# Performance work log

Hardware: AMD Instinct MI355X
Metric: run time of the kernel (lower is better)

## Reference

```python
import jax, jax.numpy as jnp
import numpy as np
from jax import lax

K = 10  # k_neighbors (k = min(k, N); N=1024 so k=10)


def setup_inputs() -> dict:
    key = jax.random.key(0)
    ks = jax.random.split(key, 6)
    B, N, M, D = 4, 1024, 8, 128
    PROJ, NC, OUT = 64, 10, 128
    x = jax.random.normal(ks[0], (B, N, M, D), dtype=jnp.float32)
    # Linear params (torch stores weight as [out, in])
    W_proj_w = jax.random.normal(ks[1], (PROJ, D), dtype=jnp.float32) / np.sqrt(D)
    W_proj_b = jnp.zeros((PROJ,), dtype=jnp.float32)
    C = jax.random.normal(ks[2], (NC, PROJ), dtype=jnp.float32) * np.sqrt(2.0 / (NC + PROJ))
    Theta_w = jax.random.normal(ks[3], (OUT, D), dtype=jnp.float32) / np.sqrt(D)
    Theta_b = jnp.zeros((OUT,), dtype=jnp.float32)
    return {"x": x, "W_proj_w": W_proj_w, "W_proj_b": W_proj_b, "C": C,
            "Theta_w": Theta_w, "Theta_b": Theta_b}


def _forward(x, W_proj_w, W_proj_b, C, Theta_w, Theta_b):
    B, N, M, D = x.shape
    BM = B * M
    x_flat = jnp.transpose(x, (0, 2, 1, 3)).reshape(BM, N, D)
    Z = x_flat @ W_proj_w.T + W_proj_b  # [BM, N, P]
    # squared euclidean pairwise distances (same topk ordering as cdist)
    sq = jnp.sum(Z * Z, axis=-1)  # [BM, N]
    d2 = sq[:, :, None] + sq[:, None, :] - 2.0 * jnp.einsum('bnp,bmp->bnm', Z, Z)
    _, idx = lax.top_k(-d2, K)  # k smallest distances -> [BM, N, K]
    # scatter 1.0 at neighbor indices
    b_ix = jnp.arange(BM)[:, None, None]
    r_ix = jnp.arange(N)[None, :, None]
    H_knn = jnp.zeros((BM, N, N), dtype=jnp.float32).at[b_ix, r_ix, idx].set(1.0)
    H_cluster = jax.nn.softmax(Z @ C.T, axis=-1)  # [BM, N, NC]
    H = jnp.concatenate([H_knn, H_cluster], axis=-1)  # [BM, N, N+NC]
    # hypergraph conv with degree normalization
    D_e = H.sum(axis=1)  # [BM, E]
    D_e_inv = jnp.where(D_e > 0, 1.0 / jnp.maximum(D_e, 1e-12), 0.0)
    D_v = H.sum(axis=2)  # [BM, N]
    D_v_inv_sqrt = jnp.where(D_v > 0, 1.0 / jnp.sqrt(jnp.maximum(D_v, 1e-12)), 0.0)
    X_trans = x_flat @ Theta_w.T + Theta_b  # [BM, N, F]
    out = D_v_inv_sqrt[:, :, None] * X_trans
    out = jnp.einsum('bne,bnf->bef', H, out)   # H^T @ out
    out = D_e_inv[:, :, None] * out
    out = jnp.einsum('bne,bef->bnf', H, out)   # H @ out
    out = D_v_inv_sqrt[:, :, None] * out
    out = jax.nn.elu(out)
    return jnp.transpose(out.reshape(B, M, N, -1), (0, 2, 1, 3))  # [B, N, M, F]


def reference(x, W_proj_w, W_proj_b, C, Theta_w, Theta_b):
    return _forward(x, W_proj_w, W_proj_b, C, Theta_w, Theta_b)
```

## Files before the change

### kernel.cpp

```cpp
#include <hip/hip_runtime.h>
#include <hip/hip_bf16.h>
#include <cstdint>
#include <cstddef>

#define BMC 32
#define NNODE 1024
#define DIN 128
#define PPROJ 64
#define NCLUS 10
#define FOUT 128
#define KNB 10

typedef _Float16 half8 __attribute__((ext_vector_type(8)));
typedef float f32x4 __attribute__((ext_vector_type(4)));

static const size_t OFF_Z    = 0;
static const size_t OFF_SQ   = 2097152;
static const size_t OFF_HC   = 2129920;
static const size_t OFF_IDX  = 2457600;
static const size_t OFF_CNT  = 2785280;
static const size_t OFF_FILL = 2818048;
static const size_t OFF_EC   = 2850816;
static const size_t OFF_DCV  = 2891776;
static const size_t OFF_OFFS = 2892096;
static const size_t OFF_ADJ  = 2924864;
static const size_t OFF_FLAG = 3252544;
static const size_t OFF_END  = 3252608;
static const size_t OFF_WPH  = OFF_EC;
static const size_t OFF_WPL  = OFF_EC +  4096;
static const size_t OFF_THH  = OFF_EC +  8192;
static const size_t OFF_THL  = OFF_EC + 16384;
static const int    ZERO2_N  = 41280;

__device__ __forceinline__ float bfu(unsigned int lo16) {
    return __uint_as_float(lo16 << 16);
}
__device__ __forceinline__ float bfhi(unsigned int w) {
    return __uint_as_float(w & 0xffff0000u);
}
__device__ __forceinline__ float ldf(const void* p, size_t i, bool isbf) {
    return isbf ? bfu((unsigned int)((const unsigned short*)p)[i])
                : ((const float*)p)[i];
}
__device__ __forceinline__ unsigned short f2bf(float v) {
    __hip_bfloat16 h = __float2bfloat16(v);
    return *(unsigned short*)&h;
}

__device__ __forceinline__ unsigned long long mkkey(float v, int col) {
    unsigned int bits = __float_as_uint(v);
    unsigned int s = bits ^ (0x80000000u | (unsigned int)((int)bits >> 31));
    return ((unsigned long long)s << 32) | (unsigned int)col;
}
__device__ __forceinline__ void kcas(unsigned long long &a, unsigned long long &b) {
    bool c = b < a;
    unsigned long long t = c ? b : a;
    b = c ? a : b;
    a = t;
}
__device__ __forceinline__ void kmin(unsigned long long &a, unsigned long long b) {
    a = (b < a) ? b : a;
}

__global__ __launch_bounds__(256) void k_probe(const unsigned int* __restrict__ xw,
                                               int* __restrict__ flag) {
    __shared__ int red[256];
    int t = threadIdx.x;
    int cnt = 0;
    for (int i = t; i < 1024; i += 256) {
        float b = bfu(xw[i] & 0xffffu);
        float ab = fabsf(b);
        if (ab > 9.5e-7f && ab < 1.0e6f) cnt++;
    }
    red[t] = cnt;
    __syncthreads();
    for (int off = 128; off > 0; off >>= 1) {
        if (t < off) red[t] += red[t + off];
        __syncthreads();
    }
    if (t == 0) flag[0] = (red[0] >= 700) ? 1 : 0;
}

__global__ __launch_bounds__(256) void k_split(const void* __restrict__ Wp,
                                               const void* __restrict__ Th,
                                               const int* __restrict__ flag,
                                               _Float16* __restrict__ WpH,
                                               _Float16* __restrict__ WpL,
                                               _Float16* __restrict__ ThH,
                                               _Float16* __restrict__ ThL,
                                               int* __restrict__ cntz) {
    const bool isbf = (flag[0] != 0);
    int i = blockIdx.x * 256 + threadIdx.x;
    cntz[i] = 0;
    if (i < 8192) cntz[i + 24576] = 0;
    if (i < 8192) {
        float v = ldf(Wp, i, isbf);
        _Float16 h = (_Float16)v;
        WpH[i] = h;
        WpL[i] = (_Float16)((v - (float)h) * 2048.0f);
    } else {
        int j = i - 8192;
        float v = ldf(Th, j, isbf);
        _Float16 h = (_Float16)v;
        ThH[j] = h;
        ThL[j] = (_Float16)((v - (float)h) * 2048.0f);
    }
}

__global__ __launch_bounds__(256) void k_proj(const void* __restrict__ x,
                                              const _Float16* __restrict__ WpH,
                                              const _Float16* __restrict__ WpL,
                                              const void* __restrict__ Wpb,
                                              const void* __restrict__ Cm,
                                              const int* __restrict__ flag,
                                              _Float16* __restrict__ Zh,
                                              _Float16* __restrict__ Zl,
                                              float* __restrict__ sqv,
                                              float* __restrict__ Hc) {
    __shared__ __align__(16) _Float16 wps[2][64][72];
    __shared__ __align__(16) _Float16 xsh[2][32][72];
    __shared__ float zs[32][68];
    __shared__ float cs[10][64];

    const bool isbf = (flag[0] != 0);
    int tid = threadIdx.x;
    int bi  = blockIdx.x;
    int bm  = bi >> 5;
    int n0  = (bi & 31) << 5;
    int b   = bm >> 3, m = bm & 7;

    int lane = tid & 63, wave = tid >> 6;
    int m16 = lane & 15, quad = lane >> 4;
    int rh = wave >> 1, ch = wave & 1;

    for (int e = tid; e < 640; e += 256) cs[e >> 6][e & 63] = ldf(Cm, e, isbf);

    f32x4 aH[2], aX[2];
#pragma unroll
    for (int t = 0; t < 2; ++t) {
        aH[t] = (f32x4){0.f, 0.f, 0.f, 0.f};
        aX[t] = (f32x4){0.f, 0.f, 0.f, 0.f};
    }

    for (int kc = 0; kc < 2; ++kc) {
        __syncthreads();
        for (int e = tid; e < 512; e += 256) {
            int p = e >> 3, c = e & 7;
            *(uint4*)&wps[0][p][c * 8] =
                *(const uint4*)(WpH + (size_t)p * 128 + kc * 64 + c * 8);
            *(uint4*)&wps[1][p][c * 8] =
                *(const uint4*)(WpL + (size_t)p * 128 + kc * 64 + c * 8);
        }
        for (int e = tid; e < 2048; e += 256) {
            int r = e >> 6, dk = e & 63;
            float v = ldf(x, (((size_t)b * NNODE + n0 + r) * 8 + m) * DIN + kc * 64 + dk, isbf);
            _Float16 h = (_Float16)v;
            xsh[0][r][dk] = h;
            xsh[1][r][dk] = (_Float16)((v - (float)h) * 2048.0f);
        }
        __syncthreads();
#pragma unroll
        for (int c32 = 0; c32 < 2; ++c32) {
            half8 Ah = *(const half8*)&xsh[0][rh * 16 + m16][c32 * 32 + quad * 8];
            half8 Al = *(const half8*)&xsh[1][rh * 16 + m16][c32 * 32 + quad * 8];
#pragma unroll
            for (int t = 0; t < 2; ++t) {
                int p = ch * 32 + t * 16 + m16;
                half8 Bh = *(const half8*)&wps[0][p][c32 * 32 + quad * 8];
                half8 Bl = *(const half8*)&wps[1][p][c32 * 32 + quad * 8];
                aH[t] = __builtin_amdgcn_mfma_f32_16x16x32_f16(Ah, Bh, aH[t], 0, 0, 0);
                aX[t] = __builtin_amdgcn_mfma_f32_16x16x32_f16(Al, Bh, aX[t], 0, 0, 0);
                aX[t] = __builtin_amdgcn_mfma_f32_16x16x32_f16(Ah, Bl, aX[t], 0, 0, 0);
            }
        }
    }

#pragma unroll
    for (int t = 0; t < 2; ++t) {
        int p = ch * 32 + t * 16 + m16;
        float bias = ldf(Wpb, p, isbf);
#pragma unroll
        for (int r = 0; r < 4; ++r) {
            int row = rh * 16 + quad * 4 + r;
            float v = aH[t][r] + aX[t][r] * (1.0f / 2048.0f) + bias;
            zs[row][p] = v;
            size_t off = ((size_t)bm * NNODE + n0 + row) * 64 + p;
            _Float16 h = (_Float16)v;
            Zh[off] = h;
            Zl[off] = (_Float16)((v - (float)h) * 2048.0f);
        }
    }
    __syncthreads();

    int row = tid >> 3, slot = tid & 7;
    int d0 = slot * 8;
    float sp = 0.f;
#pragma unroll
    for (int dd = 0; dd < 8; ++dd) { float z = zs[row][d0+dd]; sp += z * z; }
#pragma unroll
    for (int mm = 1; mm < 8; mm <<= 1) sp += __shfl_xor(sp, mm, 8);
    size_t g = (size_t)bm * NNODE + n0 + row;
    if (slot == 0) sqv[g] = sp;

    float sc[10];
#pragma unroll
    for (int c = 0; c < 10; ++c) {
        float pa = 0.f;
#pragma unroll
        for (int dd = 0; dd < 8; ++dd) pa += zs[row][d0+dd] * cs[c][d0+dd];
#pragma unroll
        for (int mm = 1; mm < 8; mm <<= 1) pa += __shfl_xor(pa, mm, 8);
        sc[c] = pa;
    }
    float mx = sc[0];
#pragma unroll
    for (int c = 1; c < 10; ++c) mx = fmaxf(mx, sc[c]);
    float ssum = 0.f;
#pragma unroll
    for (int c = 0; c < 10; ++c) { sc[c] = expf(sc[c] - mx); ssum += sc[c]; }
    float inv = 1.0f / ssum;
#pragma unroll
    for (int c = 0; c < 10; ++c)
        if ((c & 7) == slot) Hc[g * 10 + c] = sc[c] * inv;
}

__global__ __launch_bounds__(256) void k_theta(const void* __restrict__ x,
                                               const _Float16* __restrict__ ThH,
                                               const _Float16* __restrict__ ThL,
                                               const void* __restrict__ Thb,
                                               const int* __restrict__ flag,
                                               float* __restrict__ Xt) {
    __shared__ __align__(16) _Float16 ths[2][128][72];
    __shared__ __align__(16) _Float16 xsh[32][72];

    const bool isbf = (flag[0] != 0);
    int tid = threadIdx.x;
    int bi  = blockIdx.x;
    int bm  = bi >> 5;
    int n0  = (bi & 31) << 5;
    int b   = bm >> 3, m = bm & 7;

    int lane = tid & 63, wave = tid >> 6;
    int m16 = lane & 15, quad = lane >> 4;
    int rh = wave >> 1, ch = wave & 1;

    f32x4 aH[4], aX[4];
#pragma unroll
    for (int t = 0; t < 4; ++t) {
        aH[t] = (f32x4){0.f, 0.f, 0.f, 0.f};
        aX[t] = (f32x4){0.f, 0.f, 0.f, 0.f};
    }

    for (int kc = 0; kc < 2; ++kc) {
        __syncthreads();
        for (int e = tid; e < 1024; e += 256) {
            int f = e >> 3, c = e & 7;
            *(uint4*)&ths[0][f][c * 8] =
                *(const uint4*)(ThH + (size_t)f * 128 + kc * 64 + c * 8);
            *(uint4*)&ths[1][f][c * 8] =
                *(const uint4*)(ThL + (size_t)f * 128 + kc * 64 + c * 8);
        }
        for (int e = tid; e < 2048; e += 256) {
            int r = e >> 6, dk = e & 63;
            float v = ldf(x, (((size_t)b * NNODE + n0 + r) * 8 + m) * DIN + kc * 64 + dk, isbf);
            xsh[r][dk] = (_Float16)v;
        }
        __syncthreads();
#pragma unroll
        for (int c32 = 0; c32 < 2; ++c32) {
            half8 Ah = *(const half8*)&xsh[rh * 16 + m16][c32 * 32 + quad * 8];
#pragma unroll
            for (int t = 0; t < 4; ++t) {
                int f = ch * 64 + t * 16 + m16;
                half8 Bh = *(const half8*)&ths[0][f][c32 * 32 + quad * 8];
                half8 Bl = *(const half8*)&ths[1][f][c32 * 32 + quad * 8];
                aH[t] = __builtin_amdgcn_mfma_f32_16x16x32_f16(Ah, Bh, aH[t], 0, 0, 0);
                aX[t] = __builtin_amdgcn_mfma_f32_16x16x32_f16(Ah, Bl, aX[t], 0, 0, 0);
            }
        }
    }
#pragma unroll
    for (int t = 0; t < 4; ++t) {
        int f = ch * 64 + t * 16 + m16;
        float bias = ldf(Thb, f, isbf);
        size_t rb = (size_t)bm * NNODE + n0 + rh * 16 + quad * 4;
#pragma unroll
        for (int r = 0; r < 4; ++r) {
            Xt[(rb + r) * 128 + f] = aH[t][r] + aX[t][r] * (1.0f / 2048.0f) + bias;
        }
    }
}

#define TOPK_SELECT(J0)                                                        \
  {                                                                            \
    unsigned long long b0 = mkkey(ST[(sslot     ) * 36 + srow], (J0) + sslot);        \
    unsigned long long b1 = mkkey(ST[(sslot +  8) * 36 + srow], (J0) + sslot + 8);    \
    unsigned long long b2 = mkkey(ST[(sslot + 16) * 36 + srow], (J0) + sslot + 16);   \
    unsigned long long b3 = mkkey(ST[(sslot + 24) * 36 + srow], (J0) + sslot + 24);   \
    unsigned long long b4 = mkkey(ST[(sslot + 32) * 36 + srow], (J0) + sslot + 32);   \
    unsigned long long b5 = mkkey(ST[(sslot + 40) * 36 + srow], (J0) + sslot + 40);   \
    unsigned long long b6 = mkkey(ST[(sslot + 48) * 36 + srow], (J0) + sslot + 48);   \
    unsigned long long b7 = mkkey(ST[(sslot + 56) * 36 + srow], (J0) + sslot + 56);   \
    kcas(b0, b1); kcas(b2, b3); kcas(b4, b5); kcas(b6, b7);                    \
    kcas(b0, b2); kcas(b1, b3); kcas(b4, b6); kcas(b5, b7);                    \
    kcas(b1, b2); kcas(b5, b6);                                                \
    kcas(b0, b4); kcas(b1, b5); kcas(b2, b6); kcas(b3, b7);                    \
    kcas(b2, b4); kcas(b3, b5);                                                \
    kcas(b1, b2); kcas(b3, b4); kcas(b5, b6);                                  \
    kmin(keys[2], b7); kmin(keys[3], b6); kmin(keys[4], b5); kmin(keys[5], b4);\
    kmin(keys[6], b3); kmin(keys[7], b2); kmin(keys[8], b1); kmin(keys[9], b0);\
    kcas(keys[0], keys[8]); kcas(keys[1], keys[9]);                            \
    kcas(keys[2], keys[6]); kcas(keys[3], keys[7]);                            \
    kcas(keys[4], keys[8]); kcas(keys[5], keys[9]);                            \
    kcas(keys[2], keys[4]); kcas(keys[3], keys[5]);                            \
    kcas(keys[6], keys[8]); kcas(keys[7], keys[9]);                            \
    kcas(keys[0], keys[1]); kcas(keys[2], keys[3]);                            \
    kcas(keys[4], keys[5]); kcas(keys[6], keys[7]); kcas(keys[8], keys[9]);    \
  }

#define TOPK_TILE(J0, CH0,CH1,CL0,CL1,CSQ, NH0,NH1,NL0,NL1,NSQ)                \
  {                                                                            \
    f32x4 acc  = {0.f, 0.f, 0.f, 0.f};                                         \
    f32x4 accx = {0.f, 0.f, 0.f, 0.f};                                         \
    acc  = __builtin_amdgcn_mfma_f32_16x16x32_f16(ah0, CH0, acc, 0, 0, 0);     \
    acc  = __builtin_amdgcn_mfma_f32_16x16x32_f16(ah1, CH1, acc, 0, 0, 0);     \
    accx = __builtin_amdgcn_mfma_f32_16x16x32_f16(al0, CH0, accx, 0, 0, 0);    \
    accx = __builtin_amdgcn_mfma_f32_16x16x32_f16(ah0, CL0, accx, 0, 0, 0);    \
    accx = __builtin_amdgcn_mfma_f32_16x16x32_f16(al1, CH1, accx, 0, 0, 0);    \
    accx = __builtin_amdgcn_mfma_f32_16x16x32_f16(ah1, CL1, accx, 0, 0, 0);    \
    f32x4 sc;                                                                  \
    _Pragma("unroll")                                                          \
    for (int r = 0; r < 4; ++r) {                                              \
      float g = acc[r] + accx[r] * (1.0f / 2048.0f);                           \
      sc[r] = fmaf(-2.0f, g, CSQ);                                             \
    }                                                                          \
    *(f32x4*)&ST[cl * 36 + quad * 4] = sc;                                     \
    f32x4 accB  = {0.f, 0.f, 0.f, 0.f};                                        \
    f32x4 accxB = {0.f, 0.f, 0.f, 0.f};                                        \
    accB  = __builtin_amdgcn_mfma_f32_16x16x32_f16(ah0b, CH0, accB, 0, 0, 0);  \
    accB  = __builtin_amdgcn_mfma_f32_16x16x32_f16(ah1b, CH1, accB, 0, 0, 0);  \
    accxB = __builtin_amdgcn_mfma_f32_16x16x32_f16(al0b, CH0, accxB, 0, 0, 0); \
    accxB = __builtin_amdgcn_mfma_f32_16x16x32_f16(ah0b, CL0, accxB, 0, 0, 0); \
    accxB = __builtin_amdgcn_mfma_f32_16x16x32_f16(al1b, CH1, accxB, 0, 0, 0); \
    accxB = __builtin_amdgcn_mfma_f32_16x16x32_f16(ah1b, CL1, accxB, 0, 0, 0); \
    _Pragma("unroll")                                                          \
    for (int r = 0; r < 4; ++r) {                                              \
      float g = accB[r] + accxB[r] * (1.0f / 2048.0f);                         \
      sc[r] = fmaf(-2.0f, g, CSQ);                                             \
    }                                                                          \
    *(f32x4*)&ST[cl * 36 + 16 + quad * 4] = sc;                                \
    {                                                                          \
      const _Float16* pnb = Zhb + (size_t)((J0) + 64 + cl) * 64 + quad * 8;    \
      const _Float16* pnl = Zlb + (size_t)((J0) + 64 + cl) * 64 + quad * 8;    \
      NH0 = *(const half8*)pnb;                                                \
      NH1 = *(const half8*)(pnb + 32);                                         \
      NL0 = *(const half8*)pnl;                                                \
      NL1 = *(const half8*)(pnl + 32);                                         \
      NSQ = sqb[(J0) + 64 + cl];                                               \
    }                                                                          \
    asm volatile("s_waitcnt lgkmcnt(0)" ::: "memory");                         \
    __builtin_amdgcn_s_barrier();                                              \
    asm volatile("" ::: "memory");                                             \
    TOPK_SELECT(J0);                                                           \
    asm volatile("" ::: "memory");                                             \
    __builtin_amdgcn_s_barrier();                                              \
    asm volatile("" ::: "memory");                                             \
  }

__global__ __launch_bounds__(256) void k_topk(const _Float16* __restrict__ Zh,
                                              const _Float16* __restrict__ Zl,
                                              const float* __restrict__ sqv,
                                              int* __restrict__ idxo,
                                              int* __restrict__ cnt) {
    __shared__ float ST[64 * 36];

    int tid = threadIdx.x;
    int bi  = blockIdx.x;
    int bm  = bi >> 5;
    int n0  = (bi & 31) << 5;
    const _Float16* Zhb = Zh + (size_t)bm * NNODE * 64;
    const _Float16* Zlb = Zl + (size_t)bm * NNODE * 64;
    const float*    sqb = sqv + (size_t)bm * NNODE;

    int lane = tid & 63, wave = tid >> 6;
    int m16 = lane & 15, quad = lane >> 4;
    int cl = wave * 16 + m16;

    half8 ah0, ah1, al0, al1, ah0b, ah1b, al0b, al1b;
    {
        size_t ab = (size_t)(n0 + m16) * 64 + quad * 8;
        ah0 = *(const half8*)(Zhb + ab);
        ah1 = *(const half8*)(Zhb + ab + 32);
        al0 = *(const half8*)(Zlb + ab);
        al1 = *(const half8*)(Zlb + ab + 32);
        size_t ab2 = ab + 16 * 64;
        ah0b = *(const half8*)(Zhb + ab2);
        ah1b = *(const half8*)(Zhb + ab2 + 32);
        al0b = *(const half8*)(Zlb + ab2);
        al1b = *(const half8*)(Zlb + ab2 + 32);
    }

    unsigned long long keys[10];
#pragma unroll
    for (int j = 0; j < 10; ++j) keys[j] = ~0ULL;

    int srow  = tid >> 3;
    int sslot = tid & 7;

    half8 cbh0, cbh1, cbl0, cbl1, nbh0, nbh1, nbl0, nbl1;
    float csq, nsq;
    {
        const _Float16* pb = Zhb + (size_t)cl * 64 + quad * 8;
        const _Float16* pl = Zlb + (size_t)cl * 64 + quad * 8;
        cbh0 = *(const half8*)pb;
        cbh1 = *(const half8*)(pb + 32);
        cbl0 = *(const half8*)pl;
        cbl1 = *(const half8*)(pl + 32);
        csq  = sqb[cl];
    }

    for (int tp = 0; tp < 8; ++tp) {
        int j0a = tp << 7;
        TOPK_TILE(j0a,      cbh0, cbh1, cbl0, cbl1, csq, nbh0, nbh1, nbl0, nbl1, nsq)
        TOPK_TILE(j0a + 64, nbh0, nbh1, nbl0, nbl1, nsq, cbh0, cbh1, cbl0, cbl1, csq)
    }

    size_t gr = (size_t)bm * NNODE + n0 + srow;
    for (int it = 0; it < 10; ++it) {
        unsigned long long mine = keys[0];
        unsigned long long best = mine;
#pragma unroll
        for (int mm = 1; mm < 8; mm <<= 1) {
            unsigned long long o = __shfl_xor(best, mm, 8);
            if (o < best) best = o;
        }
        if (best == mine) {
#pragma unroll
            for (int j = 0; j < 9; ++j) keys[j] = keys[j+1];
            keys[9] = ~0ULL;
            int col = (int)(best & 0xFFFFFFFFu);
            idxo[gr * KNB + it] = col;
            atomicAdd(&cnt[bm * NNODE + col], 1);
        }
    }
}
#undef TOPK_TILE
#undef TOPK_SELECT

__global__ __launch_bounds__(256) void k_csr(const int* __restrict__ cnt,
                                             const int* __restrict__ idxb,
                                             int* __restrict__ offs,
                                             int* __restrict__ adj) {
    __shared__ int part[256];
    __shared__ int fillL[1024];
    int bm = blockIdx.x, t = threadIdx.x;
    int base = bm * 1024 + t * 4;
    int c0 = cnt[base], c1 = cnt[base+1], c2 = cnt[base+2], c3 = cnt[base+3];
    int ps = c0 + c1 + c2 + c3;
    part[t] = ps;
    __syncthreads();
    for (int off = 1; off < 256; off <<= 1) {
        int add = (t >= off) ? part[t - off] : 0;
        __syncthreads();
        part[t] += add;
        __syncthreads();
    }
    int e0 = part[t] - ps;
    int gb = bm * (NNODE * KNB);
    int o0 = gb + e0, o1 = o0 + c0, o2 = o1 + c1, o3 = o2 + c2;
    offs[base]   = o0;
    offs[base+1] = o1;
    offs[base+2] = o2;
    offs[base+3] = o3;
    fillL[t*4]   = o0;
    fillL[t*4+1] = o1;
    fillL[t*4+2] = o2;
    fillL[t*4+3] = o3;
    __syncthreads();
    int ibase = bm * (NNODE * KNB);
    for (int e = t; e < NNODE * KNB; e += 256) {
        int eidx = idxb[ibase + e];
        int pos = atomicAdd(&fillL[eidx], 1);
        adj[pos] = (bm << 10) + (e / 10);
    }
}

__global__ __launch_bounds__(256) void k_edge(const float* __restrict__ Xt,
                                              const int* __restrict__ offs,
                                              const int* __restrict__ cnt,
                                              const int* __restrict__ adj,
                                              unsigned short* __restrict__ Ek,
                                              float* __restrict__ EcZ) {
    int tid = threadIdx.x;
    int bi  = blockIdx.x;
    {
        int zi = bi * 256 + tid;
        if (zi < ZERO2_N) EcZ[zi] = 0.0f;
    }
    int swz = (bi & 7) * 512 + (bi >> 3);
    int e = swz * 8 + (tid >> 5);
    int l = tid & 31;
    int start = offs[e];
    int num = cnt[e];
    float4 acc = {0.f, 0.f, 0.f, 0.f};
    if (num > 0) {
        int nm1 = num - 1;
        int gidx[16];
#pragma unroll
        for (int j = 0; j < 16; ++j) {
            int jj = (j < nm1) ? j : nm1;
            gidx[j] = adj[start + jj];
        }
#pragma unroll
        for (int j = 0; j < 16; ++j) {
            float4 a = *(const float4*)(Xt + (size_t)gidx[j] * 128 + l * 4);
            float w = (j < num) ? 1.0f : 0.0f;
            acc.x = fmaf(w, a.x, acc.x);
            acc.y = fmaf(w, a.y, acc.y);
            acc.z = fmaf(w, a.z, acc.z);
            acc.w = fmaf(w, a.w, acc.w);
        }
        int i = 16;
        for (; i + 1 < num; i += 2) {
            int g0 = adj[start + i];
            int g1 = adj[start + i + 1];
            float4 a = *(const float4*)(Xt + (size_t)g0 * 128 + l * 4);
            float4 b = *(const float4*)(Xt + (size_t)g1 * 128 + l * 4);
            acc.x += a.x + b.x; acc.y += a.y + b.y;
            acc.z += a.z + b.z; acc.w += a.w + b.w;
        }
        if (i < num) {
            int g0 = adj[start + i];
            float4 a = *(const float4*)(Xt + (size_t)g0 * 128 + l * 4);
            acc.x += a.x; acc.y += a.y; acc.z += a.z; acc.w += a.w;
        }
    }
    float scale = (num > 0) ? 1.0f / (float)num : 0.0f;
    ushort4 o;
    o.x = f2bf(acc.x * scale);
    o.y = f2bf(acc.y * scale);
    o.z = f2bf(acc.z * scale);
    o.w = f2bf(acc.w * scale);
    *(ushort4*)(Ek + (size_t)e * 128 + l * 4) = o;
}

__global__ __launch_bounds__(256) void k_clus(const float* __restrict__ Xt,
                                              const float* __restrict__ Hc,
                                              float* __restrict__ Ec,
                                              float* __restrict__ Dcv) {
    __shared__ float hcs[128][12];
    int tid = threadIdx.x;
    int bm = blockIdx.x >> 3;
    int ch = blockIdx.x & 7;
    int n0 = ch * 128;

    for (int e = tid; e < 1280; e += 256) {
        int r = e / 10, c = e - r * 10;
        hcs[r][c] = Hc[((size_t)bm * NNODE + n0 + r) * 10 + c];
    }
    __syncthreads();

    int f = tid & 127;
    int h = tid >> 7;
    int c0 = h * 5;
    float acc[5]  = {0.f,0.f,0.f,0.f,0.f};
    float dacc[5] = {0.f,0.f,0.f,0.f,0.f};
#pragma unroll 2
    for (int n = 0; n < 128; ++n) {
        float xv = Xt[((size_t)bm * NNODE + n0 + n) * 128 + f];
#pragma unroll
        for (int j = 0; j < 5; ++j) {
            float hv = hcs[n][c0 + j];
            acc[j]  = fmaf(hv, xv, acc[j]);
            dacc[j] += hv;
        }
    }
#pragma unroll
    for (int j = 0; j < 5; ++j)
        atomicAdd(&Ec[((size_t)bm * 10 + c0 + j) * 128 + f], acc[j]);
    if (f == 0) {
#pragma unroll
        for (int j = 0; j < 5; ++j) atomicAdd(&Dcv[bm * 10 + c0 + j], dacc[j]);
    }
}

__global__ __launch_bounds__(256) void k_final(const unsigned short* __restrict__ Ek,
                                               const float* __restrict__ Ec,
                                               const float* __restrict__ Hc,
                                               const float* __restrict__ Dcv,
                                               const int* __restrict__ idxb,
                                               float* __restrict__ out) {
    int tid = threadIdx.x;
    int bi  = blockIdx.x;
    int swz = (bi & 7) * 512 + (bi >> 3);
    int g = swz * 8 + (tid >> 5);
    int l = tid & 31;
    int bm = g >> 10, n = g & 1023;
    const int* ip = idxb + (size_t)g * 10;
    const unsigned short* ekb = Ek + ((size_t)bm << 10) * 128 + l * 4;

    int e0 = ip[0], e1 = ip[1], e2 = ip[2], e3 = ip[3], e4 = ip[4];
    int e5 = ip[5], e6 = ip[6], e7 = ip[7], e8 = ip[8], e9 = ip[9];
    ushort4 u0 = *(const ushort4*)(ekb + (size_t)e0 * 128);
    ushort4 u1 = *(const ushort4*)(ekb + (size_t)e1 * 128);
    ushort4 u2 = *(const ushort4*)(ekb + (size_t)e2 * 128);
    ushort4 u3 = *(const ushort4*)(ekb + (size_t)e3 * 128);
    ushort4 u4 = *(const ushort4*)(ekb + (size_t)e4 * 128);
    ushort4 u5 = *(const ushort4*)(ekb + (size_t)e5 * 128);
    ushort4 u6 = *(const ushort4*)(ekb + (size_t)e6 * 128);
    ushort4 u7 = *(const ushort4*)(ekb + (size_t)e7 * 128);
    ushort4 u8 = *(const ushort4*)(ekb + (size_t)e8 * 128);
    ushort4 u9 = *(const ushort4*)(ekb + (size_t)e9 * 128);

    float4 acc;
    acc.x = bfu(u0.x) + bfu(u1.x) + bfu(u2.x) + bfu(u3.x) + bfu(u4.x)
          + bfu(u5.x) + bfu(u6.x) + bfu(u7.x) + bfu(u8.x) + bfu(u9.x);
    acc.y = bfu(u0.y) + bfu(u1.y) + bfu(u2.y) + bfu(u3.y) + bfu(u4.y)
          + bfu(u5.y) + bfu(u6.y) + bfu(u7.y) + bfu(u8.y) + bfu(u9.y);
    acc.z = bfu(u0.z) + bfu(u1.z) + bfu(u2.z) + bfu(u3.z) + bfu(u4.z)
          + bfu(u5.z) + bfu(u6.z) + bfu(u7.z) + bfu(u8.z) + bfu(u9.z);
    acc.w = bfu(u0.w) + bfu(u1.w) + bfu(u2.w) + bfu(u3.w) + bfu(u4.w)
          + bfu(u5.w) + bfu(u6.w) + bfu(u7.w) + bfu(u8.w) + bfu(u9.w);

    const float* hp  = Hc + (size_t)g * 10;
    const float* dcp = Dcv + (size_t)bm * 10;
    const float* ecp = Ec + (size_t)bm * 10 * 128 + l * 4;
#pragma unroll
    for (int c = 0; c < 10; ++c) {
        float d  = dcp[c];
        float hv = (d > 0.f) ? hp[c] / d : 0.f;
        float4 ec = *(const float4*)(ecp + c * 128);
        acc.x += hv * ec.x; acc.y += hv * ec.y;
        acc.z += hv * ec.z; acc.w += hv * ec.w;
    }
    float4 r;
    r.x = acc.x * (1.0f / 11.0f);
    r.y = acc.y * (1.0f / 11.0f);
    r.z = acc.z * (1.0f / 11.0f);
    r.w = acc.w * (1.0f / 11.0f);
    r.x = (r.x > 0.f) ? r.x : expm1f(r.x);
    r.y = (r.y > 0.f) ? r.y : expm1f(r.y);
    r.z = (r.z > 0.f) ? r.z : expm1f(r.z);
    r.w = (r.w > 0.f) ? r.w : expm1f(r.w);
    int b = bm >> 3, m = bm & 7;
    *(float4*)(out + (((size_t)b * NNODE + n) * 8 + m) * 128 + l * 4) = r;
}

extern "C" void kernel_launch(void* const* d_in, const int* in_sizes, int n_in,
                              void* d_out, int out_size, void* d_ws, size_t ws_size,
                              hipStream_t stream) {
    const void* x   = d_in[0];
    const void* Wp  = d_in[1];
    const void* Wpb = d_in[2];
    const void* Cm  = d_in[3];
    const void* Th  = d_in[4];
    const void* Thb = d_in[5];
    float* ws = (float*)d_ws;

    if (ws_size < OFF_END * sizeof(float)) return;

    _Float16* Zh = (_Float16*)(ws + OFF_Z);
    _Float16* Zl = (_Float16*)(ws + OFF_Z + 1048576);
    float* sqv  = ws + OFF_SQ;
    float* Hc   = ws + OFF_HC;
    int*   idxb = (int*)(ws + OFF_IDX);
    int*   cnt  = (int*)(ws + OFF_CNT);
    float* Ec   = ws + OFF_EC;
    float* Dcv  = ws + OFF_DCV;
    int*   offs = (int*)(ws + OFF_OFFS);
    int*   adj  = (int*)(ws + OFF_ADJ);
    int*   flag = (int*)(ws + OFF_FLAG);
    _Float16* WpH = (_Float16*)(ws + OFF_WPH);
    _Float16* WpL = (_Float16*)(ws + OFF_WPL);
    _Float16* ThH = (_Float16*)(ws + OFF_THH);
    _Float16* ThL = (_Float16*)(ws + OFF_THL);
    unsigned short* Ek = (unsigned short*)(ws + OFF_Z);
    float* Xt  = (float*)d_out;
    float* out = (float*)d_out;

    k_probe <<<1,    256, 0, stream>>>((const unsigned int*)x, flag);
    k_split <<<96,   256, 0, stream>>>(Wp, Th, flag, WpH, WpL, ThH, ThL, cnt);
    k_proj  <<<1024, 256, 0, stream>>>(x, WpH, WpL, Wpb, Cm, flag, Zh, Zl, sqv, Hc);
    k_topk  <<<1024, 256, 0, stream>>>(Zh, Zl, sqv, idxb, cnt);
    k_csr   <<<32,   256, 0, stream>>>(cnt, idxb, offs, adj);
    k_theta <<<1024, 256, 0, stream>>>(x, ThH, ThL, Thb, flag, Xt);
    k_edge  <<<4096, 256, 0, stream>>>(Xt, offs, cnt, adj, Ek, Ec);
    k_clus  <<<256,  256, 0, stream>>>(Xt, Hc, Ec, Dcv);
    k_final <<<4096, 256, 0, stream>>>(Ek, Ec, Hc, Dcv, idxb, out);
}
```

Baseline: 268.6 us.

## Halve top-k block row tile to 16 rows, doubling grid and shrinking sort network

The top-k kernel now handles 16 query rows per block instead of 32, so the grid doubles to 2048 blocks. Each row is served by 16 threads that each sort 4 candidates instead of 8 threads sorting 8, which shortens the per-thread sorting network. The shuffle reduction widens to 16 lanes to match. s_setprio is also raised around the MFMA block. The aim is more parallelism and less serial compare-swap work per thread, paid for by reloading each column tile of Z twice as often and running more barriers per useful row.

Result: slower. 290.7 us (+8.2%).

```diff
diff --git a/kernel.cpp b/kernel.cpp
--- a/kernel.cpp
+++ b/kernel.cpp
@@ -293,21 +293,13 @@
 
 #define TOPK_SELECT(J0)                                                        \
   {                                                                            \
-    unsigned long long b0 = mkkey(ST[(sslot     ) * 36 + srow], (J0) + sslot);        \
-    unsigned long long b1 = mkkey(ST[(sslot +  8) * 36 + srow], (J0) + sslot + 8);    \
-    unsigned long long b2 = mkkey(ST[(sslot + 16) * 36 + srow], (J0) + sslot + 16);   \
-    unsigned long long b3 = mkkey(ST[(sslot + 24) * 36 + srow], (J0) + sslot + 24);   \
-    unsigned long long b4 = mkkey(ST[(sslot + 32) * 36 + srow], (J0) + sslot + 32);   \
-    unsigned long long b5 = mkkey(ST[(sslot + 40) * 36 + srow], (J0) + sslot + 40);   \
-    unsigned long long b6 = mkkey(ST[(sslot + 48) * 36 + srow], (J0) + sslot + 48);   \
-    unsigned long long b7 = mkkey(ST[(sslot + 56) * 36 + srow], (J0) + sslot + 56);   \
-    kcas(b0, b1); kcas(b2, b3); kcas(b4, b5); kcas(b6, b7);                    \
-    kcas(b0, b2); kcas(b1, b3); kcas(b4, b6); kcas(b5, b7);                    \
-    kcas(b1, b2); kcas(b5, b6);                                                \
-    kcas(b0, b4); kcas(b1, b5); kcas(b2, b6); kcas(b3, b7);                    \
-    kcas(b2, b4); kcas(b3, b5);                                                \
-    kcas(b1, b2); kcas(b3, b4); kcas(b5, b6);                                  \
-    kmin(keys[2], b7); kmin(keys[3], b6); kmin(keys[4], b5); kmin(keys[5], b4);\
+    unsigned long long b0 = mkkey(ST[(sslot     ) * 20 + srow], (J0) + sslot);        \
+    unsigned long long b1 = mkkey(ST[(sslot + 16) * 20 + srow], (J0) + sslot + 16);   \
+    unsigned long long b2 = mkkey(ST[(sslot + 32) * 20 + srow], (J0) + sslot + 32);   \
+    unsigned long long b3 = mkkey(ST[(sslot + 48) * 20 + srow], (J0) + sslot + 48);   \
+    kcas(b0, b1); kcas(b2, b3);                                                \
+    kcas(b0, b2); kcas(b1, b3);                                                \
+    kcas(b1, b2);                                                              \
     kmin(keys[6], b3); kmin(keys[7], b2); kmin(keys[8], b1); kmin(keys[9], b0);\
     kcas(keys[0], keys[8]); kcas(keys[1], keys[9]);                            \
     kcas(keys[2], keys[6]); kcas(keys[3], keys[7]);                            \
@@ -320,6 +312,7 @@
 
 #define TOPK_TILE(J0, CH0,CH1,CL0,CL1,CSQ, NH0,NH1,NL0,NL1,NSQ)                \
   {                                                                            \
+    __builtin_amdgcn_s_setprio(1);                                             \
     f32x4 acc  = {0.f, 0.f, 0.f, 0.f};                                         \
     f32x4 accx = {0.f, 0.f, 0.f, 0.f};                                         \
     acc  = __builtin_amdgcn_mfma_f32_16x16x32_f16(ah0, CH0, acc, 0, 0, 0);     \
@@ -328,27 +321,14 @@
     accx = __builtin_amdgcn_mfma_f32_16x16x32_f16(ah0, CL0, accx, 0, 0, 0);    \
     accx = __builtin_amdgcn_mfma_f32_16x16x32_f16(al1, CH1, accx, 0, 0, 0);    \
     accx = __builtin_amdgcn_mfma_f32_16x16x32_f16(ah1, CL1, accx, 0, 0, 0);    \
+    __builtin_amdgcn_s_setprio(0);                                             \
     f32x4 sc;                                                                  \
     _Pragma("unroll")                                                          \
     for (int r = 0; r < 4; ++r) {                                              \
       float g = acc[r] + accx[r] * (1.0f / 2048.0f);                           \
       sc[r] = fmaf(-2.0f, g, CSQ);                                             \
     }                                                                          \
-    *(f32x4*)&ST[cl * 36 + quad * 4] = sc;                                     \
-    f32x4 accB  = {0.f, 0.f, 0.f, 0.f};                                        \
-    f32x4 accxB = {0.f, 0.f, 0.f, 0.f};                                        \
-    accB  = __builtin_amdgcn_mfma_f32_16x16x32_f16(ah0b, CH0, accB, 0, 0, 0);  \
-    accB  = __builtin_amdgcn_mfma_f32_16x16x32_f16(ah1b, CH1, accB, 0, 0, 0);  \
-    accxB = __builtin_amdgcn_mfma_f32_16x16x32_f16(al0b, CH0, accxB, 0, 0, 0); \
-    accxB = __builtin_amdgcn_mfma_f32_16x16x32_f16(ah0b, CL0, accxB, 0, 0, 0); \
-    accxB = __builtin_amdgcn_mfma_f32_16x16x32_f16(al1b, CH1, accxB, 0, 0, 0); \
-    accxB = __builtin_amdgcn_mfma_f32_16x16x32_f16(ah1b, CL1, accxB, 0, 0, 0); \
-    _Pragma("unroll")                                                          \
-    for (int r = 0; r < 4; ++r) {                                              \
-      float g = accB[r] + accxB[r] * (1.0f / 2048.0f);                         \
-      sc[r] = fmaf(-2.0f, g, CSQ);                                             \
-    }                                                                          \
-    *(f32x4*)&ST[cl * 36 + 16 + quad * 4] = sc;                                \
+    *(f32x4*)&ST[cl * 20 + quad * 4] = sc;                                     \
     {                                                                          \
       const _Float16* pnb = Zhb + (size_t)((J0) + 64 + cl) * 64 + quad * 8;    \
       const _Float16* pnl = Zlb + (size_t)((J0) + 64 + cl) * 64 + quad * 8;    \
@@ -372,12 +352,12 @@
                                               const float* __restrict__ sqv,
                                               int* __restrict__ idxo,
                                               int* __restrict__ cnt) {
-    __shared__ float ST[64 * 36];
+    __shared__ float ST[64 * 20];
 
     int tid = threadIdx.x;
     int bi  = blockIdx.x;
-    int bm  = bi >> 5;
-    int n0  = (bi & 31) << 5;
+    int bm  = bi >> 6;
+    int n0  = (bi & 63) << 4;
     const _Float16* Zhb = Zh + (size_t)bm * NNODE * 64;
     const _Float16* Zlb = Zl + (size_t)bm * NNODE * 64;
     const float*    sqb = sqv + (size_t)bm * NNODE;
@@ -386,26 +366,21 @@
     int m16 = lane & 15, quad = lane >> 4;
     int cl = wave * 16 + m16;
 
-    half8 ah0, ah1, al0, al1, ah0b, ah1b, al0b, al1b;
+    half8 ah0, ah1, al0, al1;
     {
         size_t ab = (size_t)(n0 + m16) * 64 + quad * 8;
         ah0 = *(const half8*)(Zhb + ab);
         ah1 = *(const half8*)(Zhb + ab + 32);
         al0 = *(const half8*)(Zlb + ab);
         al1 = *(const half8*)(Zlb + ab + 32);
-        size_t ab2 = ab + 16 * 64;
-        ah0b = *(const half8*)(Zhb + ab2);
-        ah1b = *(const half8*)(Zhb + ab2 + 32);
-        al0b = *(const half8*)(Zlb + ab2);
-        al1b = *(const half8*)(Zlb + ab2 + 32);
     }
 
     unsigned long long keys[10];
 #pragma unroll
     for (int j = 0; j < 10; ++j) keys[j] = ~0ULL;
 
-    int srow  = tid >> 3;
-    int sslot = tid & 7;
+    int srow  = tid >> 4;
+    int sslot = tid & 15;
 
     half8 cbh0, cbh1, cbl0, cbl1, nbh0, nbh1, nbl0, nbl1;
     float csq, nsq;
@@ -430,8 +405,8 @@
         unsigned long long mine = keys[0];
         unsigned long long best = mine;
 #pragma unroll
-        for (int mm = 1; mm < 8; mm <<= 1) {
-            unsigned long long o = __shfl_xor(best, mm, 8);
+        for (int mm = 1; mm < 16; mm <<= 1) {
+            unsigned long long o = __shfl_xor(best, mm, 16);
             if (o < best) best = o;
         }
         if (best == mine) {
@@ -681,7 +656,7 @@
     k_probe <<<1,    256, 0, stream>>>((const unsigned int*)x, flag);
     k_split <<<96,   256, 0, stream>>>(Wp, Th, flag, WpH, WpL, ThH, ThL, cnt);
     k_proj  <<<1024, 256, 0, stream>>>(x, WpH, WpL, Wpb, Cm, flag, Zh, Zl, sqv, Hc);
-    k_topk  <<<1024, 256, 0, stream>>>(Zh, Zl, sqv, idxb, cnt);
+    k_topk  <<<2048, 256, 0, stream>>>(Zh, Zl, sqv, idxb, cnt);
     k_csr   <<<32,   256, 0, stream>>>(cnt, idxb, offs, adj);
     k_theta <<<1024, 256, 0, stream>>>(x, ThH, ThL, Thb, flag, Xt);
     k_edge  <<<4096, 256, 0, stream>>>(Xt, offs, cnt, adj, Ek, Ec);
```

## Merge probe into split kernel and fuse cluster aggregation into edge kernel

Applied to the files above, without the earlier changes.

The dtype probe is folded into k_split: every block recomputes the reduction and block 0 writes the flag. The Ec/Dcv zeroing moves from k_edge into k_split, and the split weights are relocated into the fill scratch area so the zeroing does not clobber them. k_clus becomes the first 256 blocks of a combined k_edgeclus launch. This cuts two kernel launches and their serialization gaps. The cost is redundant probe work in every split block and mixed block types in one grid.

Result: faster. 252.1 us (-6.1%).

```diff
diff --git a/kernel.cpp b/kernel.cpp
--- a/kernel.cpp
+++ b/kernel.cpp
@@ -26,11 +26,10 @@
 static const size_t OFF_ADJ  = 2924864;
 static const size_t OFF_FLAG = 3252544;
 static const size_t OFF_END  = 3252608;
-static const size_t OFF_WPH  = OFF_EC;
-static const size_t OFF_WPL  = OFF_EC +  4096;
-static const size_t OFF_THH  = OFF_EC +  8192;
-static const size_t OFF_THL  = OFF_EC + 16384;
-static const int    ZERO2_N  = 41280;
+static const size_t OFF_WPH  = OFF_FILL;
+static const size_t OFF_WPL  = OFF_FILL +  4096;
+static const size_t OFF_THH  = OFF_FILL +  8192;
+static const size_t OFF_THL  = OFF_FILL + 16384;
 
 __device__ __forceinline__ float bfu(unsigned int lo16) {
     return __uint_as_float(lo16 << 16);
@@ -62,37 +61,39 @@
     a = (b < a) ? b : a;
 }
 
-__global__ __launch_bounds__(256) void k_probe(const unsigned int* __restrict__ xw,
-                                               int* __restrict__ flag) {
-    __shared__ int red[256];
-    int t = threadIdx.x;
-    int cnt = 0;
-    for (int i = t; i < 1024; i += 256) {
-        float b = bfu(xw[i] & 0xffffu);
-        float ab = fabsf(b);
-        if (ab > 9.5e-7f && ab < 1.0e6f) cnt++;
-    }
-    red[t] = cnt;
-    __syncthreads();
-    for (int off = 128; off > 0; off >>= 1) {
-        if (t < off) red[t] += red[t + off];
-        __syncthreads();
-    }
-    if (t == 0) flag[0] = (red[0] >= 700) ? 1 : 0;
-}
-
-__global__ __launch_bounds__(256) void k_split(const void* __restrict__ Wp,
+__global__ __launch_bounds__(256) void k_split(const unsigned int* __restrict__ xw,
+                                               const void* __restrict__ Wp,
                                                const void* __restrict__ Th,
-                                               const int* __restrict__ flag,
+                                               int* __restrict__ flag,
                                                _Float16* __restrict__ WpH,
                                                _Float16* __restrict__ WpL,
                                                _Float16* __restrict__ ThH,
                                                _Float16* __restrict__ ThL,
-                                               int* __restrict__ cntz) {
-    const bool isbf = (flag[0] != 0);
-    int i = blockIdx.x * 256 + threadIdx.x;
+                                               int* __restrict__ cntz,
+                                               float* __restrict__ EcZ) {
+    __shared__ int red[256];
+    int t = threadIdx.x;
+    int c = 0;
+    for (int i = t; i < 1024; i += 256) {
+        float b = bfu(xw[i] & 0xffffu);
+        float ab = fabsf(b);
+        if (ab > 9.5e-7f && ab < 1.0e6f) c++;
+    }
+    red[t] = c;
+    __syncthreads();
+    for (int off = 128; off > 0; off >>= 1) {
+        if (t < off) red[t] += red[t + off];
+        __syncthreads();
+    }
+    const bool isbf = (red[0] >= 700);
+    if (blockIdx.x == 0 && t == 0) flag[0] = isbf ? 1 : 0;
+
+    int i = blockIdx.x * 256 + t;
     cntz[i] = 0;
     if (i < 8192) cntz[i + 24576] = 0;
+    EcZ[i] = 0.0f;
+    if (i < 16704) EcZ[i + 24576] = 0.0f;
+
     if (i < 8192) {
         float v = ldf(Wp, i, isbf);
         _Float16 h = (_Float16)v;
@@ -485,19 +486,56 @@
     }
 }
 
-__global__ __launch_bounds__(256) void k_edge(const float* __restrict__ Xt,
-                                              const int* __restrict__ offs,
-                                              const int* __restrict__ cnt,
-                                              const int* __restrict__ adj,
-                                              unsigned short* __restrict__ Ek,
-                                              float* __restrict__ EcZ) {
+__global__ __launch_bounds__(256) void k_edgeclus(const float* __restrict__ Xt,
+                                                  const int* __restrict__ offs,
+                                                  const int* __restrict__ cnt,
+                                                  const int* __restrict__ adj,
+                                                  unsigned short* __restrict__ Ek,
+                                                  const float* __restrict__ Hc,
+                                                  float* __restrict__ Ec,
+                                                  float* __restrict__ Dcv) {
+    __shared__ float hcs[128][12];
     int tid = threadIdx.x;
     int bi  = blockIdx.x;
-    {
-        int zi = bi * 256 + tid;
-        if (zi < ZERO2_N) EcZ[zi] = 0.0f;
-    }
-    int swz = (bi & 7) * 512 + (bi >> 3);
+
+    if (bi < 256) {
+        int bm = bi >> 3;
+        int ch = bi & 7;
+        int n0 = ch * 128;
+
+        for (int e = tid; e < 1280; e += 256) {
+            int r = e / 10, c = e - r * 10;
+            hcs[r][c] = Hc[((size_t)bm * NNODE + n0 + r) * 10 + c];
+        }
+        __syncthreads();
+
+        int f = tid & 127;
+        int h = tid >> 7;
+        int c0 = h * 5;
+        float acc[5]  = {0.f,0.f,0.f,0.f,0.f};
+        float dacc[5] = {0.f,0.f,0.f,0.f,0.f};
+#pragma unroll 2
+        for (int n = 0; n < 128; ++n) {
+            float xv = Xt[((size_t)bm * NNODE + n0 + n) * 128 + f];
+#pragma unroll
+            for (int j = 0; j < 5; ++j) {
+                float hv = hcs[n][c0 + j];
+                acc[j]  = fmaf(hv, xv, acc[j]);
+                dacc[j] += hv;
+            }
+        }
+#pragma unroll
+        for (int j = 0; j < 5; ++j)
+            atomicAdd(&Ec[((size_t)bm * 10 + c0 + j) * 128 + f], acc[j]);
+        if (f == 0) {
+#pragma unroll
+            for (int j = 0; j < 5; ++j) atomicAdd(&Dcv[bm * 10 + c0 + j], dacc[j]);
+        }
+        return;
+    }
+
+    int ebi = bi - 256;
+    int swz = (ebi & 7) * 512 + (ebi >> 3);
     int e = swz * 8 + (tid >> 5);
     int l = tid & 31;
     int start = offs[e];
@@ -542,46 +580,6 @@
     o.z = f2bf(acc.z * scale);
     o.w = f2bf(acc.w * scale);
     *(ushort4*)(Ek + (size_t)e * 128 + l * 4) = o;
-}
-
-__global__ __launch_bounds__(256) void k_clus(const float* __restrict__ Xt,
-                                              const float* __restrict__ Hc,
-                                              float* __restrict__ Ec,
-                                              float* __restrict__ Dcv) {
-    __shared__ float hcs[128][12];
-    int tid = threadIdx.x;
-    int bm = blockIdx.x >> 3;
-    int ch = blockIdx.x & 7;
-    int n0 = ch * 128;
-
-    for (int e = tid; e < 1280; e += 256) {
-        int r = e / 10, c = e - r * 10;
-        hcs[r][c] = Hc[((size_t)bm * NNODE + n0 + r) * 10 + c];
-    }
-    __syncthreads();
-
-    int f = tid & 127;
-    int h = tid >> 7;
-    int c0 = h * 5;
-    float acc[5]  = {0.f,0.f,0.f,0.f,0.f};
-    float dacc[5] = {0.f,0.f,0.f,0.f,0.f};
-#pragma unroll 2
-    for (int n = 0; n < 128; ++n) {
-        float xv = Xt[((size_t)bm * NNODE + n0 + n) * 128 + f];
-#pragma unroll
-        for (int j = 0; j < 5; ++j) {
-            float hv = hcs[n][c0 + j];
-            acc[j]  = fmaf(hv, xv, acc[j]);
-            dacc[j] += hv;
-        }
-    }
-#pragma unroll
-    for (int j = 0; j < 5; ++j)
-        atomicAdd(&Ec[((size_t)bm * 10 + c0 + j) * 128 + f], acc[j]);
-    if (f == 0) {
-#pragma unroll
-        for (int j = 0; j < 5; ++j) atomicAdd(&Dcv[bm * 10 + c0 + j], dacc[j]);
-    }
 }
 
 __global__ __launch_bounds__(256) void k_final(const unsigned short* __restrict__ Ek,
@@ -678,13 +676,12 @@
     float* Xt  = (float*)d_out;
     float* out = (float*)d_out;
 
-    k_probe <<<1,    256, 0, stream>>>((const unsigned int*)x, flag);
-    k_split <<<96,   256, 0, stream>>>(Wp, Th, flag, WpH, WpL, ThH, ThL, cnt);
-    k_proj  <<<1024, 256, 0, stream>>>(x, WpH, WpL, Wpb, Cm, flag, Zh, Zl, sqv, Hc);
-    k_topk  <<<1024, 256, 0, stream>>>(Zh, Zl, sqv, idxb, cnt);
-    k_csr   <<<32,   256, 0, stream>>>(cnt, idxb, offs, adj);
-    k_theta <<<1024, 256, 0, stream>>>(x, ThH, ThL, Thb, flag, Xt);
-    k_edge  <<<4096, 256, 0, stream>>>(Xt, offs, cnt, adj, Ek, Ec);
-    k_clus  <<<256,  256, 0, stream>>>(Xt, Hc, Ec, Dcv);
-    k_final <<<4096, 256, 0, stream>>>(Ek, Ec, Hc, Dcv, idxb, out);
-}
+    k_split   <<<96,   256, 0, stream>>>((const unsigned int*)x, Wp, Th, flag,
+                                         WpH, WpL, ThH, ThL, cnt, Ec);
+    k_proj    <<<1024, 256, 0, stream>>>(x, WpH, WpL, Wpb, Cm, flag, Zh, Zl, sqv, Hc);
+    k_topk    <<<1024, 256, 0, stream>>>(Zh, Zl, sqv, idxb, cnt);
+    k_csr     <<<32,   256, 0, stream>>>(cnt, idxb, offs, adj);
+    k_theta   <<<1024, 256, 0, stream>>>(x, ThH, ThL, Thb, flag, Xt);
+    k_edgeclus<<<4352, 256, 0, stream>>>(Xt, offs, cnt, adj, Ek, Hc, Ec, Dcv);
+    k_final   <<<4096, 256, 0, stream>>>(Ek, Ec, Hc, Dcv, idxb, out);
+}
```
